# Kernel tuning notes

Measured on AMD Instinct MI355X. Metric: run time of the kernel, lower is better.

## Reference

```python
import jax, jax.numpy as jnp
import numpy as np

N_NODES = 100000
N_EDGES = 1600000
IN_F, HID, EMB = 128, 64, 32


def setup_inputs() -> dict:
    key = jax.random.key(0)
    ks = jax.random.split(key, 10)
    x = jax.random.normal(ks[0], (N_NODES, IN_F), dtype=jnp.float32)
    edge_index = jax.random.randint(ks[1], (2, N_EDGES), 0, N_NODES, dtype=jnp.int64)
    s = lambda k, sh, fan_in: jax.random.normal(k, sh, dtype=jnp.float32) / jnp.sqrt(jnp.float32(fan_in))
    return {
        "x": x,
        "edge_index": edge_index,
        # SAGEConv1: lin_l (applied to aggregated neighbors, with bias) + lin_r (root, no bias)
        "W1_l": s(ks[2], (IN_F, HID), IN_F), "b1": jnp.zeros((HID,), jnp.float32), "W1_r": s(ks[3], (IN_F, HID), IN_F),
        # SAGEConv2
        "W2_l": s(ks[4], (HID, EMB), HID), "b2": jnp.zeros((EMB,), jnp.float32), "W2_r": s(ks[5], (HID, EMB), HID),
        # risk head
        "Wh": s(ks[6], (EMB, 1), EMB), "bh": jnp.zeros((1,), jnp.float32),
    }


def _sage_conv(x, src, dst, W_l, b, W_r):
    # gather messages from source nodes, segment-mean at destination nodes
    msg_sum = jax.ops.segment_sum(x[src], dst, num_segments=N_NODES)  # [N, F]
    cnt = jax.ops.segment_sum(jnp.ones((src.shape[0],), x.dtype), dst, num_segments=N_NODES)
    mean_agg = msg_sum / jnp.maximum(cnt, 1.0)[:, None]  # isolated nodes -> 0
    return mean_agg @ W_l + b + x @ W_r


def reference(x, edge_index, W1_l, b1, W1_r, W2_l, b2, W2_r, Wh, bh):
    src, dst = edge_index[0], edge_index[1]
    h = jax.nn.relu(_sage_conv(x, src, dst, W1_l, b1, W1_r))
    # dropout is identity in eval mode
    embeddings = jax.nn.relu(_sage_conv(h, src, dst, W2_l, b2, W2_r))
    risk_scores = embeddings @ Wh + bh
    return embeddings, risk_scores
```

## Files before the change

kernel.cpp:

```cpp
#include <hip/hip_runtime.h>
#include <hip/hip_bf16.h>

#define N_NODES 100000
#define N_EDGES 1600000
#define NBUCK   782
#define BSHIFT  7
#define BCAP    3072

typedef __bf16 bf16x8 __attribute__((ext_vector_type(8)));
typedef float  f32x4  __attribute__((ext_vector_type(4)));
typedef float  f32x2  __attribute__((ext_vector_type(2)));


__device__ inline unsigned char enc_fp8(float v) {
    return (unsigned char)(__builtin_amdgcn_cvt_pk_fp8_f32(v, v, 0, 0) & 0xFF);
}

__device__ inline void gemm1_tile(const __bf16* Bt, const float* __restrict__ x,
                                  unsigned char* __restrict__ c1l,
                                  __bf16* __restrict__ c1r,
                                  int mbase, int lane, int wave) {
    int col  = lane & 15;
    int kgrp = (lane >> 4) << 3;
    int mrow = mbase + wave * 16 + col;
    int mclamp = mrow < N_NODES ? mrow : N_NODES - 1;
    const float* arow = x + (size_t)mclamp * 128;

    f32x4 acc[8];
#pragma unroll
    for (int i = 0; i < 8; ++i) acc[i] = (f32x4){0.f, 0.f, 0.f, 0.f};

#pragma unroll
    for (int ks = 0; ks < 4; ++ks) {
        int kk = ks * 32 + kgrp;
        f32x4 a0 = *(const f32x4*)(arow + kk);
        f32x4 a1 = *(const f32x4*)(arow + kk + 4);
        bf16x8 a;
#pragma unroll
        for (int i = 0; i < 4; ++i) { a[i] = (__bf16)a0[i]; a[i + 4] = (__bf16)a1[i]; }
#pragma unroll
        for (int nt = 0; nt < 8; ++nt) {
            bf16x8 b = *(const bf16x8*)(Bt + (nt * 16 + col) * 136 + kk);
            acc[nt] = __builtin_amdgcn_mfma_f32_16x16x32_bf16(a, b, acc[nt], 0, 0, 0);
        }
    }

    int r0 = mbase + wave * 16 + ((lane >> 4) << 2);
#pragma unroll
    for (int r = 0; r < 4; ++r) {
        int m = r0 + r;
        if (m < N_NODES) {
#pragma unroll
            for (int nt = 0; nt < 4; ++nt)
                c1l[(size_t)m * 64 + nt * 16 + col] = enc_fp8(acc[nt][r]);
#pragma unroll
            for (int nt = 4; nt < 8; ++nt)
                c1r[(size_t)m * 64 + (nt - 4) * 16 + col] = (__bf16)acc[nt][r];
        }
    }
}

__device__ inline void stage_W1(__bf16* Bt, const float* __restrict__ W1l,
                                const float* __restrict__ W1r, int t) {
    for (int idx = t; idx < 8192; idx += 256) {
        int k = idx >> 6, n = idx & 63;
        Bt[n * 136 + k]        = (__bf16)W1l[idx];
        Bt[(n + 64) * 136 + k] = (__bf16)W1r[idx];
    }
}

__global__ __launch_bounds__(256) void part_gemm1a_k(const int* __restrict__ ei,
                                                     int* __restrict__ gcur,
                                                     unsigned* __restrict__ bbuf,
                                                     const float* __restrict__ x,
                                                     const float* __restrict__ W1l,
                                                     const float* __restrict__ W1r,
                                                     unsigned char* __restrict__ c1l,
                                                     __bf16* __restrict__ c1r) {
    __shared__ __align__(16) char smem[34816];
    int t = threadIdx.x;
    if (blockIdx.x < 391) {
        int* hist = (int*)smem;
        int* cur  = (int*)(smem + 3328);
        for (int i = t; i < NBUCK; i += 256) hist[i] = 0;
        __syncthreads();
        int base = blockIdx.x * 4096;
        unsigned pk[16];
        int bk[16];
#pragma unroll
        for (int i = 0; i < 16; ++i) {
            int e = base + t + i * 256;
            if (e < N_EDGES) {
                int s = ei[e], d = ei[N_EDGES + e];
                int b = d >> BSHIFT;
                pk[i] = ((unsigned)(d & 127) << 17) | (unsigned)s;
                bk[i] = b;
                atomicAdd(&hist[b], 1);
            } else bk[i] = -1;
        }
        __syncthreads();
        for (int i = t; i < NBUCK; i += 256)
            cur[i] = atomicAdd(&gcur[i], hist[i]);
        __syncthreads();
#pragma unroll
        for (int i = 0; i < 16; ++i) {
            if (bk[i] >= 0) {
                int pos = atomicAdd(&cur[bk[i]], 1);
                bbuf[(size_t)bk[i] * BCAP + pos] = pk[i];
            }
        }
    } else {
        __bf16* Bt = (__bf16*)smem;
        stage_W1(Bt, W1l, W1r, t);
        __syncthreads();
        int mbase = (blockIdx.x - 391) * 64;
        gemm1_tile(Bt, x, c1l, c1r, mbase, t & 63, t >> 6);
    }
}

__global__ __launch_bounds__(256) void csr_gemm1b_k(const unsigned* __restrict__ bbuf,
                                                    const int* __restrict__ gcur,
                                                    int* __restrict__ cnt,
                                                    int* __restrict__ offsets,
                                                    int* __restrict__ csr,
                                                    const float* __restrict__ x,
                                                    const float* __restrict__ W1l,
                                                    const float* __restrict__ W1r,
                                                    unsigned char* __restrict__ c1l,
                                                    __bf16* __restrict__ c1r) {
    __shared__ __align__(16) char smem[34816];
    int t = threadIdx.x;
    if (blockIdx.x < NBUCK) {
        int* lcnt = (int*)smem;
        int* lcur = (int*)(smem + 512);
        int* ssum = (int*)(smem + 1024);
        int b = blockIdx.x;
        int m = gcur[b];
        const unsigned* src = bbuf + (size_t)b * BCAP;
        if (t < 128) lcnt[t] = 0;
        __syncthreads();
        for (int i = t; i < m; i += 256) atomicAdd(&lcnt[src[i] >> 17], 1);
        __syncthreads();
        int a0 = 0;
        if (t < 128) { a0 = lcnt[t]; ssum[t] = (a0 + 3) & ~3; }
        __syncthreads();
        for (int off = 1; off < 128; off <<= 1) {
            int v = (t < 128 && t >= off) ? ssum[t - off] : 0;
            __syncthreads();
            if (t < 128) ssum[t] += v;
            __syncthreads();
        }
        if (t < 128) {
            int ebase = (t == 0) ? 0 : ssum[t - 1];
            lcur[t] = ebase;
            int n = (b << BSHIFT) + t;
            if (n < N_NODES) {
                cnt[n] = a0;
                offsets[n] = b * BCAP + ebase;
            }
        }
        __syncthreads();
        for (int i = t; i < m; i += 256) {
            unsigned p = src[i];
            int pos = atomicAdd(&lcur[p >> 17], 1);
            csr[(size_t)b * BCAP + pos] = (int)(p & 0x1FFFF);
        }
    } else {
        __bf16* Bt = (__bf16*)smem;
        stage_W1(Bt, W1l, W1r, t);
        __syncthreads();
        int mbase = 50048 + (blockIdx.x - NBUCK) * 64;
        gemm1_tile(Bt, x, c1l, c1r, mbase, t & 63, t >> 6);
    }
}

__global__ __launch_bounds__(256) void agg1_gemm2_k(const unsigned char* __restrict__ c1l,
                                                    const __bf16* __restrict__ c1r,
                                                    const int* __restrict__ offsets,
                                                    const int* __restrict__ cnt,
                                                    const int* __restrict__ csr,
                                                    const float* __restrict__ b1,
                                                    const float* __restrict__ W2l,
                                                    const float* __restrict__ W2r,
                                                    unsigned char* __restrict__ c2l,
                                                    float* __restrict__ c2r) {
    __shared__ __bf16 Bt[64 * 72];
    __shared__ __bf16 ht[64 * 76];
    int tid = threadIdx.x;
    for (int idx = tid; idx < 2048; idx += 256) {
        int k = idx >> 5, n = idx & 31;
        Bt[n * 72 + k]        = (__bf16)W2l[idx];
        Bt[(n + 32) * 72 + k] = (__bf16)W2r[idx];
    }

    int lane = tid & 63, wave = tid >> 6;
    int g = lane >> 3;
    int f8b = (lane & 7) << 3;
    f32x4 b1v0 = *(const f32x4*)(b1 + f8b);
    f32x4 b1v1 = *(const f32x4*)(b1 + f8b + 4);
    const int4* csr4 = (const int4*)csr;
#pragma unroll
    for (int p = 0; p < 2; ++p) {
        int lrow = p * 32 + wave * 8 + g;
        int n = blockIdx.x * 64 + lrow;
        bf16x8 o;
        if (n < N_NODES) {
            int beg = offsets[n], deg = cnt[n];
            int end = beg + deg;
            bf16x8 rv = *(const bf16x8*)(c1r + (size_t)n * 64 + f8b);
            int4 j0 = csr4[beg >> 2];
            int4 j1 = csr4[(beg >> 2) + 1];
            float sum[8];
#pragma unroll
            for (int j = 0; j < 8; ++j) sum[j] = 0.f;
            for (int e = beg; e < end; e += 8) {
                int4 i0 = j0, i1 = j1;
                j0 = csr4[(e >> 2) + 2];
                j1 = csr4[(e >> 2) + 3];
                int sidx[8] = {i0.x, i0.y, i0.z, i0.w, i1.x, i1.y, i1.z, i1.w};
                uint2 w[8];
#pragma unroll
                for (int u = 0; u < 8; ++u) {
                    w[u].x = 0u; w[u].y = 0u;
                    if (e + u < end)
                        w[u] = *(const uint2*)(c1l + (size_t)sidx[u] * 64 + f8b);
                }
#pragma unroll
                for (int u = 0; u < 8; ++u) {
                    f32x2 p0 = __builtin_amdgcn_cvt_pk_f32_fp8(w[u].x, 0);
                    f32x2 p1 = __builtin_amdgcn_cvt_pk_f32_fp8(w[u].x, 1);
                    f32x2 p2 = __builtin_amdgcn_cvt_pk_f32_fp8(w[u].y, 0);
                    f32x2 p3 = __builtin_amdgcn_cvt_pk_f32_fp8(w[u].y, 1);
                    sum[0] += p0[0]; sum[1] += p0[1];
                    sum[2] += p1[0]; sum[3] += p1[1];
                    sum[4] += p2[0]; sum[5] += p2[1];
                    sum[6] += p3[0]; sum[7] += p3[1];
                }
            }
            float cf = deg > 0 ? (float)deg : 1.f;
#pragma unroll
            for (int j = 0; j < 8; ++j) {
                float v = sum[j] / cf + (float)rv[j] + ((j < 4) ? b1v0[j] : b1v1[j - 4]);
                o[j] = (__bf16)(v > 0.f ? v : 0.f);
            }
        } else {
#pragma unroll
            for (int j = 0; j < 8; ++j) o[j] = (__bf16)0.f;
        }
        *(bf16x8*)(ht + lrow * 76 + f8b) = o;
    }
    __syncthreads();

    int col  = lane & 15;
    int kgrp = (lane >> 4) << 3;
    int mbase = blockIdx.x * 64 + wave * 16;
    const __bf16* arow = ht + (wave * 16 + col) * 76;

    f32x4 acc[4];
#pragma unroll
    for (int i = 0; i < 4; ++i) acc[i] = (f32x4){0.f, 0.f, 0.f, 0.f};

#pragma unroll
    for (int ks = 0; ks < 2; ++ks) {
        int kk = ks * 32 + kgrp;
        bf16x8 a = *(const bf16x8*)(arow + kk);
#pragma unroll
        for (int nt = 0; nt < 4; ++nt) {
            bf16x8 b = *(const bf16x8*)(Bt + (nt * 16 + col) * 72 + kk);
            acc[nt] = __builtin_amdgcn_mfma_f32_16x16x32_bf16(a, b, acc[nt], 0, 0, 0);
        }
    }

    int r0 = mbase + ((lane >> 4) << 2);
#pragma unroll
    for (int r = 0; r < 4; ++r) {
        int m = r0 + r;
        if (m < N_NODES) {
#pragma unroll
            for (int nt = 0; nt < 2; ++nt)
                c2l[(size_t)m * 32 + nt * 16 + col] = enc_fp8(acc[nt][r]);
#pragma unroll
            for (int nt = 2; nt < 4; ++nt)
                c2r[(size_t)m * 32 + (nt - 2) * 16 + col] = acc[nt][r];
        }
    }
}

__global__ __launch_bounds__(256) void agg2_k(const unsigned char* __restrict__ c2l,
                                              const float* __restrict__ c2r,
                                              const int* __restrict__ offsets,
                                              const int* __restrict__ cnt,
                                              const int* __restrict__ csr,
                                              const float* __restrict__ b2,
                                              const float* __restrict__ Wh,
                                              const float* __restrict__ bh,
                                              float* __restrict__ out) {
    int wave = blockIdx.x * 4 + (threadIdx.x >> 6);
    int lane = threadIdx.x & 63;
    int g = lane >> 2;
    int n = wave * 16 + g;
    int f8b = (lane & 3) << 3;
    bool valid = n < N_NODES;
    int nc = valid ? n : N_NODES - 1;
    int beg = offsets[nc], deg = valid ? cnt[n] : 0;
    int end = beg + deg;
    f32x4 rr0 = *(const f32x4*)(c2r + (size_t)nc * 32 + f8b);
    f32x4 rr1 = *(const f32x4*)(c2r + (size_t)nc * 32 + f8b + 4);
    f32x4 wh0 = *(const f32x4*)(Wh + f8b);
    f32x4 wh1 = *(const f32x4*)(Wh + f8b + 4);
    const int4* csr4 = (const int4*)csr;
    int4 j0 = csr4[beg >> 2];
    int4 j1 = csr4[(beg >> 2) + 1];
    float sum[8];
#pragma unroll
    for (int j = 0; j < 8; ++j) sum[j] = 0.f;
    for (int e = beg; e < end; e += 8) {
        int4 i0 = j0, i1 = j1;
        j0 = csr4[(e >> 2) + 2];
        j1 = csr4[(e >> 2) + 3];
        int sidx[8] = {i0.x, i0.y, i0.z, i0.w, i1.x, i1.y, i1.z, i1.w};
        uint2 w[8];
#pragma unroll
        for (int u = 0; u < 8; ++u) {
            w[u].x = 0u; w[u].y = 0u;
            if (e + u < end)
                w[u] = *(const uint2*)(c2l + (size_t)sidx[u] * 32 + f8b);
        }
#pragma unroll
        for (int u = 0; u < 8; ++u) {
            f32x2 p0 = __builtin_amdgcn_cvt_pk_f32_fp8(w[u].x, 0);
            f32x2 p1 = __builtin_amdgcn_cvt_pk_f32_fp8(w[u].x, 1);
            f32x2 p2 = __builtin_amdgcn_cvt_pk_f32_fp8(w[u].y, 0);
            f32x2 p3 = __builtin_amdgcn_cvt_pk_f32_fp8(w[u].y, 1);
            sum[0] += p0[0]; sum[1] += p0[1];
            sum[2] += p1[0]; sum[3] += p1[1];
            sum[4] += p2[0]; sum[5] += p2[1];
            sum[6] += p3[0]; sum[7] += p3[1];
        }
    }
    float cf = deg > 0 ? (float)deg : 1.f;
    float r = 0.f;
    f32x4 o0, o1;
#pragma unroll
    for (int j = 0; j < 8; ++j) {
        float root = (j < 4) ? rr0[j] : rr1[j - 4];
        float whj  = (j < 4) ? wh0[j] : wh1[j - 4];
        float v = sum[j] / cf + root + b2[f8b + j];
        v = v > 0.f ? v : 0.f;
        if (j < 4) o0[j] = v; else o1[j - 4] = v;
        r += v * whj;
    }
    if (valid) {
        *(f32x4*)(out + (size_t)n * 32 + f8b) = o0;
        *(f32x4*)(out + (size_t)n * 32 + f8b + 4) = o1;
    }
    r += __shfl_xor(r, 1, 64);
    r += __shfl_xor(r, 2, 64);
    if (valid && (lane & 3) == 0)
        out[(size_t)N_NODES * 32 + n] = r + bh[0];
}

extern "C" void kernel_launch(void* const* d_in, const int* in_sizes, int n_in,
                              void* d_out, int out_size, void* d_ws, size_t ws_size,
                              hipStream_t stream) {
    const float* x   = (const float*)d_in[0];
    const int*   ei  = (const int*)d_in[1];
    const float* W1l = (const float*)d_in[2];
    const float* b1  = (const float*)d_in[3];
    const float* W1r = (const float*)d_in[4];
    const float* W2l = (const float*)d_in[5];
    const float* b2  = (const float*)d_in[6];
    const float* W2r = (const float*)d_in[7];
    const float* Wh  = (const float*)d_in[8];
    const float* bh  = (const float*)d_in[9];
    float* out = (float*)d_out;

    char* ws = (char*)d_ws;
    unsigned char* c1l = (unsigned char*)(ws);
    __bf16*   c1r     = (__bf16*)(ws + 6400000);
    unsigned char* c2l = (unsigned char*)(ws + 32000000);
    float*    c2r     = (float*)(ws + 35200000);
    int*      cnt     = (int*)(ws + 48000000);
    int*      offsets = (int*)(ws + 48400000);
    int*      gcur    = (int*)(ws + 48800000);
    unsigned* bbuf    = (unsigned*)(ws + 48804096);
    int*      csr     = (int*)(ws + 58437888);

    hipMemsetAsync(gcur, 0, NBUCK * 4, stream);

    part_gemm1a_k<<<391 + 782, 256, 0, stream>>>(ei, gcur, bbuf,
                                                 x, W1l, W1r, c1l, c1r);
    csr_gemm1b_k <<<NBUCK + 781, 256, 0, stream>>>(bbuf, gcur, cnt, offsets, csr,
                                                   x, W1l, W1r, c1l, c1r);
    agg1_gemm2_k <<<1563, 256, 0, stream>>>(c1l, c1r, offsets, cnt, csr, b1,
                                            W2l, W2r, c2l, c2r);
    agg2_k       <<<1563, 256, 0, stream>>>(c2l, c2r, offsets, cnt, csr, b2, Wh, bh, out);
}
```

Before: 204.1 us.

## Fuse all stages into one persistent cooperative kernel with grid syncs

Result: slower. 475.6 us (+133.0%).

```diff
diff --git a/kernel.cpp b/kernel.cpp
--- a/kernel.cpp
+++ b/kernel.cpp
@@ -1,11 +1,17 @@
 #include <hip/hip_runtime.h>
 #include <hip/hip_bf16.h>
+#include <hip/hip_cooperative_groups.h>
+
+namespace cg = cooperative_groups;
 
 #define N_NODES 100000
 #define N_EDGES 1600000
 #define NBUCK   782
 #define BSHIFT  7
 #define BCAP    3072
+#define P_UNITS 391
+#define G1_UNITS 1563
+#define AG_UNITS 1563
 
 typedef __bf16 bf16x8 __attribute__((ext_vector_type(8)));
 typedef float  f32x4  __attribute__((ext_vector_type(4)));
@@ -16,10 +22,98 @@
     return (unsigned char)(__builtin_amdgcn_cvt_pk_fp8_f32(v, v, 0, 0) & 0xFF);
 }
 
-__device__ inline void gemm1_tile(const __bf16* Bt, const float* __restrict__ x,
+__device__ inline void partition_unit(int ub, const int* __restrict__ ei,
+                                      int* __restrict__ gcur,
+                                      unsigned* __restrict__ bbuf,
+                                      char* smem, int t) {
+    int* hist = (int*)smem;
+    int* cur  = (int*)(smem + 3328);
+    for (int i = t; i < NBUCK; i += 256) hist[i] = 0;
+    __syncthreads();
+    int base = ub * 4096;
+    unsigned pk[16];
+    int bk[16];
+#pragma unroll
+    for (int i = 0; i < 16; ++i) {
+        int e = base + t + i * 256;
+        if (e < N_EDGES) {
+            int s = ei[e], d = ei[N_EDGES + e];
+            int b = d >> BSHIFT;
+            pk[i] = ((unsigned)(d & 127) << 17) | (unsigned)s;
+            bk[i] = b;
+            atomicAdd(&hist[b], 1);
+        } else bk[i] = -1;
+    }
+    __syncthreads();
+    for (int i = t; i < NBUCK; i += 256)
+        cur[i] = atomicAdd(&gcur[i], hist[i]);
+    __syncthreads();
+#pragma unroll
+    for (int i = 0; i < 16; ++i) {
+        if (bk[i] >= 0) {
+            int pos = atomicAdd(&cur[bk[i]], 1);
+            bbuf[(size_t)bk[i] * BCAP + pos] = pk[i];
+        }
+    }
+}
+
+__device__ inline void csr_unit(int b, const unsigned* __restrict__ bbuf,
+                                const int* __restrict__ gcur,
+                                int* __restrict__ cnt,
+                                int* __restrict__ offsets,
+                                int* __restrict__ csr,
+                                char* smem, int t) {
+    int* lcnt = (int*)smem;
+    int* lcur = (int*)(smem + 512);
+    int* ssum = (int*)(smem + 1024);
+    int m = gcur[b];
+    const unsigned* src = bbuf + (size_t)b * BCAP;
+    if (t < 128) lcnt[t] = 0;
+    __syncthreads();
+    for (int i = t; i < m; i += 256) atomicAdd(&lcnt[src[i] >> 17], 1);
+    __syncthreads();
+    int a0 = 0;
+    if (t < 128) { a0 = lcnt[t]; ssum[t] = (a0 + 3) & ~3; }
+    __syncthreads();
+    for (int off = 1; off < 128; off <<= 1) {
+        int v = (t < 128 && t >= off) ? ssum[t - off] : 0;
+        __syncthreads();
+        if (t < 128) ssum[t] += v;
+        __syncthreads();
+    }
+    if (t < 128) {
+        int ebase = (t == 0) ? 0 : ssum[t - 1];
+        lcur[t] = ebase;
+        int n = (b << BSHIFT) + t;
+        if (n < N_NODES) {
+            cnt[n] = a0;
+            offsets[n] = b * BCAP + ebase;
+        }
+    }
+    __syncthreads();
+    for (int i = t; i < m; i += 256) {
+        unsigned p = src[i];
+        int pos = atomicAdd(&lcur[p >> 17], 1);
+        csr[(size_t)b * BCAP + pos] = (int)(p & 0x1FFFF);
+    }
+}
+
+__device__ inline void gemm1_unit(int ub, const float* __restrict__ x,
+                                  const float* __restrict__ W1l,
+                                  const float* __restrict__ W1r,
                                   unsigned char* __restrict__ c1l,
                                   __bf16* __restrict__ c1r,
-                                  int mbase, int lane, int wave) {
+                                  char* smem, int t) {
+    __bf16* Bt = (__bf16*)smem;
+    for (int idx = t; idx < 8192; idx += 256) {
+        int k = idx >> 6, n = idx & 63;
+        Bt[n * 136 + k]        = (__bf16)W1l[idx];
+        Bt[(n + 64) * 136 + k] = (__bf16)W1r[idx];
+    }
+    __syncthreads();
+
+    int lane = t & 63, wave = t >> 6;
+    int mbase = ub * 64;
     int col  = lane & 15;
     int kgrp = (lane >> 4) << 3;
     int mrow = mbase + wave * 16 + col;
@@ -60,140 +154,26 @@
     }
 }
 
-__device__ inline void stage_W1(__bf16* Bt, const float* __restrict__ W1l,
-                                const float* __restrict__ W1r, int t) {
-    for (int idx = t; idx < 8192; idx += 256) {
-        int k = idx >> 6, n = idx & 63;
-        Bt[n * 136 + k]        = (__bf16)W1l[idx];
-        Bt[(n + 64) * 136 + k] = (__bf16)W1r[idx];
-    }
-}
-
-__global__ __launch_bounds__(256) void part_gemm1a_k(const int* __restrict__ ei,
-                                                     int* __restrict__ gcur,
-                                                     unsigned* __restrict__ bbuf,
-                                                     const float* __restrict__ x,
-                                                     const float* __restrict__ W1l,
-                                                     const float* __restrict__ W1r,
-                                                     unsigned char* __restrict__ c1l,
-                                                     __bf16* __restrict__ c1r) {
-    __shared__ __align__(16) char smem[34816];
-    int t = threadIdx.x;
-    if (blockIdx.x < 391) {
-        int* hist = (int*)smem;
-        int* cur  = (int*)(smem + 3328);
-        for (int i = t; i < NBUCK; i += 256) hist[i] = 0;
-        __syncthreads();
-        int base = blockIdx.x * 4096;
-        unsigned pk[16];
-        int bk[16];
-#pragma unroll
-        for (int i = 0; i < 16; ++i) {
-            int e = base + t + i * 256;
-            if (e < N_EDGES) {
-                int s = ei[e], d = ei[N_EDGES + e];
-                int b = d >> BSHIFT;
-                pk[i] = ((unsigned)(d & 127) << 17) | (unsigned)s;
-                bk[i] = b;
-                atomicAdd(&hist[b], 1);
-            } else bk[i] = -1;
-        }
-        __syncthreads();
-        for (int i = t; i < NBUCK; i += 256)
-            cur[i] = atomicAdd(&gcur[i], hist[i]);
-        __syncthreads();
-#pragma unroll
-        for (int i = 0; i < 16; ++i) {
-            if (bk[i] >= 0) {
-                int pos = atomicAdd(&cur[bk[i]], 1);
-                bbuf[(size_t)bk[i] * BCAP + pos] = pk[i];
-            }
-        }
-    } else {
-        __bf16* Bt = (__bf16*)smem;
-        stage_W1(Bt, W1l, W1r, t);
-        __syncthreads();
-        int mbase = (blockIdx.x - 391) * 64;
-        gemm1_tile(Bt, x, c1l, c1r, mbase, t & 63, t >> 6);
-    }
-}
-
-__global__ __launch_bounds__(256) void csr_gemm1b_k(const unsigned* __restrict__ bbuf,
-                                                    const int* __restrict__ gcur,
-                                                    int* __restrict__ cnt,
-                                                    int* __restrict__ offsets,
-                                                    int* __restrict__ csr,
-                                                    const float* __restrict__ x,
-                                                    const float* __restrict__ W1l,
-                                                    const float* __restrict__ W1r,
-                                                    unsigned char* __restrict__ c1l,
-                                                    __bf16* __restrict__ c1r) {
-    __shared__ __align__(16) char smem[34816];
-    int t = threadIdx.x;
-    if (blockIdx.x < NBUCK) {
-        int* lcnt = (int*)smem;
-        int* lcur = (int*)(smem + 512);
-        int* ssum = (int*)(smem + 1024);
-        int b = blockIdx.x;
-        int m = gcur[b];
-        const unsigned* src = bbuf + (size_t)b * BCAP;
-        if (t < 128) lcnt[t] = 0;
-        __syncthreads();
-        for (int i = t; i < m; i += 256) atomicAdd(&lcnt[src[i] >> 17], 1);
-        __syncthreads();
-        int a0 = 0;
-        if (t < 128) { a0 = lcnt[t]; ssum[t] = (a0 + 3) & ~3; }
-        __syncthreads();
-        for (int off = 1; off < 128; off <<= 1) {
-            int v = (t < 128 && t >= off) ? ssum[t - off] : 0;
-            __syncthreads();
-            if (t < 128) ssum[t] += v;
-            __syncthreads();
-        }
-        if (t < 128) {
-            int ebase = (t == 0) ? 0 : ssum[t - 1];
-            lcur[t] = ebase;
-            int n = (b << BSHIFT) + t;
-            if (n < N_NODES) {
-                cnt[n] = a0;
-                offsets[n] = b * BCAP + ebase;
-            }
-        }
-        __syncthreads();
-        for (int i = t; i < m; i += 256) {
-            unsigned p = src[i];
-            int pos = atomicAdd(&lcur[p >> 17], 1);
-            csr[(size_t)b * BCAP + pos] = (int)(p & 0x1FFFF);
-        }
-    } else {
-        __bf16* Bt = (__bf16*)smem;
-        stage_W1(Bt, W1l, W1r, t);
-        __syncthreads();
-        int mbase = 50048 + (blockIdx.x - NBUCK) * 64;
-        gemm1_tile(Bt, x, c1l, c1r, mbase, t & 63, t >> 6);
-    }
-}
-
-__global__ __launch_bounds__(256) void agg1_gemm2_k(const unsigned char* __restrict__ c1l,
-                                                    const __bf16* __restrict__ c1r,
-                                                    const int* __restrict__ offsets,
-                                                    const int* __restrict__ cnt,
-                                                    const int* __restrict__ csr,
-                                                    const float* __restrict__ b1,
-                                                    const float* __restrict__ W2l,
-                                                    const float* __restrict__ W2r,
-                                                    unsigned char* __restrict__ c2l,
-                                                    float* __restrict__ c2r) {
-    __shared__ __bf16 Bt[64 * 72];
-    __shared__ __bf16 ht[64 * 76];
-    int tid = threadIdx.x;
-    for (int idx = tid; idx < 2048; idx += 256) {
+__device__ inline void agg1_gemm2_unit(int ub, const unsigned char* __restrict__ c1l,
+                                       const __bf16* __restrict__ c1r,
+                                       const int* __restrict__ offsets,
+                                       const int* __restrict__ cnt,
+                                       const int* __restrict__ csr,
+                                       const float* __restrict__ b1,
+                                       const float* __restrict__ W2l,
+                                       const float* __restrict__ W2r,
+                                       unsigned char* __restrict__ c2l,
+                                       float* __restrict__ c2r,
+                                       char* smem, int t) {
+    __bf16* Bt = (__bf16*)smem;
+    __bf16* ht = (__bf16*)(smem + 9216);
+    for (int idx = t; idx < 2048; idx += 256) {
         int k = idx >> 5, n = idx & 31;
         Bt[n * 72 + k]        = (__bf16)W2l[idx];
         Bt[(n + 32) * 72 + k] = (__bf16)W2r[idx];
     }
 
-    int lane = tid & 63, wave = tid >> 6;
+    int lane = t & 63, wave = t >> 6;
     int g = lane >> 3;
     int f8b = (lane & 7) << 3;
     f32x4 b1v0 = *(const f32x4*)(b1 + f8b);
@@ -202,7 +182,7 @@
 #pragma unroll
     for (int p = 0; p < 2; ++p) {
         int lrow = p * 32 + wave * 8 + g;
-        int n = blockIdx.x * 64 + lrow;
+        int n = ub * 64 + lrow;
         bf16x8 o;
         if (n < N_NODES) {
             int beg = offsets[n], deg = cnt[n];
@@ -253,7 +233,7 @@
 
     int col  = lane & 15;
     int kgrp = (lane >> 4) << 3;
-    int mbase = blockIdx.x * 64 + wave * 16;
+    int mbase = ub * 64 + wave * 16;
     const __bf16* arow = ht + (wave * 16 + col) * 76;
 
     f32x4 acc[4];
@@ -286,17 +266,17 @@
     }
 }
 
-__global__ __launch_bounds__(256) void agg2_k(const unsigned char* __restrict__ c2l,
-                                              const float* __restrict__ c2r,
-                                              const int* __restrict__ offsets,
-                                              const int* __restrict__ cnt,
-                                              const int* __restrict__ csr,
-                                              const float* __restrict__ b2,
-                                              const float* __restrict__ Wh,
-                                              const float* __restrict__ bh,
-                                              float* __restrict__ out) {
-    int wave = blockIdx.x * 4 + (threadIdx.x >> 6);
-    int lane = threadIdx.x & 63;
+__device__ inline void agg2_unit(int ub, const unsigned char* __restrict__ c2l,
+                                 const float* __restrict__ c2r,
+                                 const int* __restrict__ offsets,
+                                 const int* __restrict__ cnt,
+                                 const int* __restrict__ csr,
+                                 const float* __restrict__ b2,
+                                 const float* __restrict__ Wh,
+                                 const float* __restrict__ bh,
+                                 float* __restrict__ out, int t) {
+    int wave = ub * 4 + (t >> 6);
+    int lane = t & 63;
     int g = lane >> 2;
     int n = wave * 16 + g;
     int f8b = (lane & 3) << 3;
@@ -360,6 +340,116 @@
         out[(size_t)N_NODES * 32 + n] = r + bh[0];
 }
 
+__global__ __launch_bounds__(256, 4) void fused_k(
+        const int* __restrict__ ei,
+        int* __restrict__ gcur,
+        unsigned* __restrict__ bbuf,
+        int* __restrict__ cnt,
+        int* __restrict__ offsets,
+        int* __restrict__ csr,
+        const float* __restrict__ x,
+        const float* __restrict__ W1l,
+        const float* __restrict__ W1r,
+        const float* __restrict__ b1,
+        const float* __restrict__ W2l,
+        const float* __restrict__ W2r,
+        const float* __restrict__ b2,
+        const float* __restrict__ Wh,
+        const float* __restrict__ bh,
+        unsigned char* __restrict__ c1l,
+        __bf16* __restrict__ c1r,
+        unsigned char* __restrict__ c2l,
+        float* __restrict__ c2r,
+        float* __restrict__ out) {
+    cg::grid_group grid = cg::this_grid();
+    __shared__ __align__(16) char smem[34816];
+    int t = threadIdx.x;
+    int gsz = gridDim.x;
+
+    for (int i = blockIdx.x * 256 + t; i < NBUCK; i += gsz * 256) gcur[i] = 0;
+    grid.sync();
+
+    for (int vb = blockIdx.x; vb < P_UNITS + 782; vb += gsz) {
+        __syncthreads();
+        if (vb < P_UNITS) partition_unit(vb, ei, gcur, bbuf, smem, t);
+        else              gemm1_unit(vb - P_UNITS, x, W1l, W1r, c1l, c1r, smem, t);
+    }
+    grid.sync();
+
+    for (int vb = blockIdx.x; vb < G1_UNITS; vb += gsz) {
+        __syncthreads();
+        if (vb < NBUCK) csr_unit(vb, bbuf, gcur, cnt, offsets, csr, smem, t);
+        else            gemm1_unit(vb, x, W1l, W1r, c1l, c1r, smem, t);
+    }
+    grid.sync();
+
+    for (int vb = blockIdx.x; vb < AG_UNITS; vb += gsz) {
+        __syncthreads();
+        agg1_gemm2_unit(vb, c1l, c1r, offsets, cnt, csr, b1, W2l, W2r, c2l, c2r, smem, t);
+    }
+    grid.sync();
+
+    for (int vb = blockIdx.x; vb < AG_UNITS; vb += gsz)
+        agg2_unit(vb, c2l, c2r, offsets, cnt, csr, b2, Wh, bh, out, t);
+}
+
+__global__ __launch_bounds__(256) void part_gemm1a_k(const int* __restrict__ ei,
+                                                     int* __restrict__ gcur,
+                                                     unsigned* __restrict__ bbuf,
+                                                     const float* __restrict__ x,
+                                                     const float* __restrict__ W1l,
+                                                     const float* __restrict__ W1r,
+                                                     unsigned char* __restrict__ c1l,
+                                                     __bf16* __restrict__ c1r) {
+    __shared__ __align__(16) char smem[34816];
+    int t = threadIdx.x;
+    if (blockIdx.x < P_UNITS) partition_unit(blockIdx.x, ei, gcur, bbuf, smem, t);
+    else                      gemm1_unit(blockIdx.x - P_UNITS, x, W1l, W1r, c1l, c1r, smem, t);
+}
+
+__global__ __launch_bounds__(256) void csr_gemm1b_k(const unsigned* __restrict__ bbuf,
+                                                    const int* __restrict__ gcur,
+                                                    int* __restrict__ cnt,
+                                                    int* __restrict__ offsets,
+                                                    int* __restrict__ csr,
+                                                    const float* __restrict__ x,
+                                                    const float* __restrict__ W1l,
+                                                    const float* __restrict__ W1r,
+                                                    unsigned char* __restrict__ c1l,
+                                                    __bf16* __restrict__ c1r) {
+    __shared__ __align__(16) char smem[34816];
+    int t = threadIdx.x;
+    if (blockIdx.x < NBUCK) csr_unit(blockIdx.x, bbuf, gcur, cnt, offsets, csr, smem, t);
+    else                    gemm1_unit(blockIdx.x, x, W1l, W1r, c1l, c1r, smem, t);
+}
+
+__global__ __launch_bounds__(256) void agg1_gemm2_k(const unsigned char* __restrict__ c1l,
+                                                    const __bf16* __restrict__ c1r,
+                                                    const int* __restrict__ offsets,
+                                                    const int* __restrict__ cnt,
+                                                    const int* __restrict__ csr,
+                                                    const float* __restrict__ b1,
+                                                    const float* __restrict__ W2l,
+                                                    const float* __restrict__ W2r,
+                                                    unsigned char* __restrict__ c2l,
+                                                    float* __restrict__ c2r) {
+    __shared__ __align__(16) char smem[34816];
+    agg1_gemm2_unit(blockIdx.x, c1l, c1r, offsets, cnt, csr, b1, W2l, W2r,
+                    c2l, c2r, smem, threadIdx.x);
+}
+
+__global__ __launch_bounds__(256) void agg2_k(const unsigned char* __restrict__ c2l,
+                                              const float* __restrict__ c2r,
+                                              const int* __restrict__ offsets,
+                                              const int* __restrict__ cnt,
+                                              const int* __restrict__ csr,
+                                              const float* __restrict__ b2,
+                                              const float* __restrict__ Wh,
+                                              const float* __restrict__ bh,
+                                              float* __restrict__ out) {
+    agg2_unit(blockIdx.x, c2l, c2r, offsets, cnt, csr, b2, Wh, bh, out, threadIdx.x);
+}
+
 extern "C" void kernel_launch(void* const* d_in, const int* in_sizes, int n_in,
                               void* d_out, int out_size, void* d_ws, size_t ws_size,
                               hipStream_t stream) {
@@ -386,13 +476,38 @@
     unsigned* bbuf    = (unsigned*)(ws + 48804096);
     int*      csr     = (int*)(ws + 58437888);
 
-    hipMemsetAsync(gcur, 0, NBUCK * 4, stream);
-
-    part_gemm1a_k<<<391 + 782, 256, 0, stream>>>(ei, gcur, bbuf,
-                                                 x, W1l, W1r, c1l, c1r);
-    csr_gemm1b_k <<<NBUCK + 781, 256, 0, stream>>>(bbuf, gcur, cnt, offsets, csr,
-                                                   x, W1l, W1r, c1l, c1r);
-    agg1_gemm2_k <<<1563, 256, 0, stream>>>(c1l, c1r, offsets, cnt, csr, b1,
-                                            W2l, W2r, c2l, c2r);
-    agg2_k       <<<1563, 256, 0, stream>>>(c2l, c2r, offsets, cnt, csr, b2, Wh, bh, out);
-}
+    static int grid_blocks = 0;
+    if (grid_blocks == 0) {
+        int mb = 0, ncu = 0;
+        if (hipOccupancyMaxActiveBlocksPerMultiprocessor(&mb, (const void*)fused_k,
+                                                         256, 0) != hipSuccess || mb <= 0)
+            mb = 2;
+        if (hipDeviceGetAttribute(&ncu, hipDeviceAttributeMultiprocessorCount, 0)
+                != hipSuccess || ncu <= 0)
+            ncu = 256;
+        long g = (long)mb * (long)ncu;
+        if (g > G1_UNITS) g = G1_UNITS;
+        grid_blocks = (int)g;
+    }
+
+    void* args[] = {
+        (void*)&ei, (void*)&gcur, (void*)&bbuf, (void*)&cnt, (void*)&offsets,
+        (void*)&csr, (void*)&x, (void*)&W1l, (void*)&W1r, (void*)&b1,
+        (void*)&W2l, (void*)&W2r, (void*)&b2, (void*)&Wh, (void*)&bh,
+        (void*)&c1l, (void*)&c1r, (void*)&c2l, (void*)&c2r, (void*)&out
+    };
+    hipError_t err = hipLaunchCooperativeKernel((const void*)fused_k,
+                                                dim3(grid_blocks), dim3(256),
+                                                args, 0, stream);
+    if (err != hipSuccess) {
+        hipMemsetAsync(gcur, 0, NBUCK * 4, stream);
+        part_gemm1a_k<<<P_UNITS + 782, 256, 0, stream>>>(ei, gcur, bbuf,
+                                                         x, W1l, W1r, c1l, c1r);
+        csr_gemm1b_k <<<NBUCK + 781, 256, 0, stream>>>(bbuf, gcur, cnt, offsets, csr,
+                                                       x, W1l, W1r, c1l, c1r);
+        agg1_gemm2_k <<<AG_UNITS, 256, 0, stream>>>(c1l, c1r, offsets, cnt, csr, b1,
+                                                    W2l, W2r, c2l, c2r);
+        agg2_k       <<<AG_UNITS, 256, 0, stream>>>(c2l, c2r, offsets, cnt, csr,
+                                                    b2, Wh, bh, out);
+    }
+}
```
